# Optimization experiments

Measured on AMD Instinct MI355X. Metric: run time of the kernel, lower is better.

## Reference

```python
import jax, jax.numpy as jnp
import numpy as np

B, M, N, Z = 4, 64, 64, 64
IN_DIM, OUT_DIM = 32, 32
MODES1 = MODES2 = MODES3 = 16
HIDDEN = OUT_DIM * 4  # factor=4, n_ff_layers=2
LN_EPS = 1e-5


def setup_inputs() -> dict:
    key = jax.random.key(0)
    ks = jax.random.split(key, 10)
    # xavier-normal-ish scale for (in, out, modes, 2) fourier weights
    fscale = np.sqrt(2.0 / (IN_DIM + OUT_DIM))
    x = jax.random.normal(ks[0], (B, M, N, Z, IN_DIM), dtype=jnp.float32)
    wx = jax.random.normal(ks[1], (IN_DIM, OUT_DIM, MODES1, 2), dtype=jnp.float32) * fscale
    wy = jax.random.normal(ks[2], (IN_DIM, OUT_DIM, MODES2, 2), dtype=jnp.float32) * fscale
    wz = jax.random.normal(ks[3], (IN_DIM, OUT_DIM, MODES3, 2), dtype=jnp.float32) * fscale
    # FeedForward: Linear(OUT_DIM, HIDDEN) + ReLU, then Linear(HIDDEN, OUT_DIM) + LayerNorm
    w0 = jax.random.normal(ks[4], (OUT_DIM, HIDDEN), dtype=jnp.float32) * np.sqrt(1.0 / OUT_DIM)
    b0 = jnp.zeros((HIDDEN,), dtype=jnp.float32)
    w1 = jax.random.normal(ks[5], (HIDDEN, OUT_DIM), dtype=jnp.float32) * np.sqrt(1.0 / HIDDEN)
    b1 = jnp.zeros((OUT_DIM,), dtype=jnp.float32)
    ln_g = jnp.ones((OUT_DIM,), dtype=jnp.float32)
    ln_b = jnp.zeros((OUT_DIM,), dtype=jnp.float32)
    return {"x": x, "wx": wx, "wy": wy, "wz": wz,
            "w0": w0, "b0": b0, "w1": w1, "b1": b1,
            "ln_g": ln_g, "ln_b": ln_b}


def _as_complex(w):
    return w[..., 0] + 1j * w[..., 1]


def _forward_fourier(x, wx, wy, wz):
    # x: [b, m, n, z, i] -> [b, i, m, n, z]
    xt = jnp.transpose(x, (0, 4, 1, 2, 3))
    # --- axis M (dim 2) ---
    ftx = jnp.fft.rfft(xt, axis=2, norm='ortho')  # [b, i, M//2+1, n, z] complex
    ox = jnp.einsum('bixyz,iox->boxyz', ftx[:, :, :MODES1], _as_complex(wx))
    ox = jnp.pad(ox, ((0, 0), (0, 0), (0, M // 2 + 1 - MODES1), (0, 0), (0, 0)))
    xx = jnp.fft.irfft(ox, n=M, axis=2, norm='ortho')
    # --- axis N (dim 3) ---
    fty = jnp.fft.rfft(xt, axis=3, norm='ortho')
    oy = jnp.einsum('bixyz,ioy->boxyz', fty[:, :, :, :MODES2], _as_complex(wy))
    oy = jnp.pad(oy, ((0, 0), (0, 0), (0, 0), (0, N // 2 + 1 - MODES2), (0, 0)))
    xy = jnp.fft.irfft(oy, n=N, axis=3, norm='ortho')
    # --- axis Z (dim 4) ---
    ftz = jnp.fft.rfft(xt, axis=4, norm='ortho')
    oz = jnp.einsum('bixyz,ioz->boxyz', ftz[:, :, :, :, :MODES3], _as_complex(wz))
    oz = jnp.pad(oz, ((0, 0), (0, 0), (0, 0), (0, 0), (0, Z // 2 + 1 - MODES3)))
    xz = jnp.fft.irfft(oz, n=Z, axis=4, norm='ortho')
    out = xx + xy + xz  # [b, o, m, n, z]
    return jnp.transpose(out, (0, 2, 3, 4, 1))  # [b, m, n, z, o]


def reference(x, wx, wy, wz, w0, b0, w1, b1, ln_g, ln_b):
    s = _forward_fourier(x, wx, wy, wz)
    h = jax.nn.relu(s @ w0 + b0)
    y = h @ w1 + b1
    mu = jnp.mean(y, axis=-1, keepdims=True)
    var = jnp.mean((y - mu) ** 2, axis=-1, keepdims=True)
    y = (y - mu) * jax.lax.rsqrt(var + LN_EPS) * ln_g + ln_b
    return y
```

## Files before the change

### kernel.cpp

```cpp
#include <hip/hip_runtime.h>
#include <math.h>

typedef __attribute__((ext_vector_type(8))) short short8v;
typedef __attribute__((ext_vector_type(4))) float float4v;

constexpr float THETA = 6.28318530717958647692f / 64.0f;

constexpr int S_B = 64 * 64 * 64 * 32;
constexpr int S_M = 64 * 64 * 32;
constexpr int S_N = 64 * 32;
constexpr int S_Z = 32;

__device__ __forceinline__ unsigned short f2bf(float f) {
    unsigned int u = __builtin_bit_cast(unsigned int, f);
    u += 0x7FFFu + ((u >> 16) & 1u);
    return (unsigned short)(u >> 16);
}

constexpr int WS_TF = 98304, WS_TI = 100352, WS_TOTAL = 102400;

__global__ __launch_bounds__(256)
void setup_frags(const float* __restrict__ wx, const float* __restrict__ wy,
                 const float* __restrict__ wz, unsigned short* __restrict__ W)
{
    int f0 = (blockIdx.x * 256 + threadIdx.x) * 4;
#pragma unroll
    for (int u = 0; u < 4; ++u) {
        int f = f0 + u;
        if (f >= WS_TOTAL) continue;
        unsigned short v;
        if (f < WS_TF) {
            int ax = f >> 15, rem = f & 32767;
            int k = rem >> 11;
            int rem2 = rem & 2047;
            int wt = rem2 >> 10, rt = (rem2 >> 9) & 1, l = (rem2 >> 3) & 63, e = rem2 & 7;
            int o = 16 * rt + (l & 15), i = 8 * (l >> 4) + e;
            const float* w = (ax == 0) ? wx : ((ax == 1) ? wy : wz);
            v = f2bf(w[((i * 32 + o) * 16 + k) * 2 + wt]);
        } else if (f < WS_TI) {
            int rem = f - WS_TF;
            int jt = rem >> 10, s = (rem >> 9) & 1, l = (rem >> 3) & 63, e = rem & 7;
            int kk = l & 15, m = 32 * s + 8 * (l >> 4) + e;
            int jm = (kk * m) & 63;
            float ang = THETA * (float)jm;
            v = f2bf(jt == 0 ? cosf(ang) : sinf(ang));
        } else {
            int rem = f - WS_TI;
            int mt = rem >> 9, l = (rem >> 3) & 63, e = rem & 7;
            int mp = 16 * mt + (l & 15), r = 8 * (l >> 4) + e;
            int k = r & 15;
            float sk = (k == 0) ? (1.0f / 64.0f) : (2.0f / 64.0f);
            int jm = (k * mp) & 63;
            float ang = THETA * (float)jm;
            v = f2bf(r < 16 ? sk * cosf(ang) : -sk * sinf(ang));
        }
        W[f] = v;
    }
}

constexpr int AB_SHORTS = 8192;
__device__ __forceinline__ int ab8(int t, int k, int line, int i) {
    return ((((t * 16 + k) * 8 + line) * 64) + i * 2) ^ (((line ^ k) & 7) << 4);
}
constexpr int P_LS = 1288;
constexpr int P_SHORTS = 8 * P_LS;
__device__ __forceinline__ int p8(int line, int o, int r) {
    return line * P_LS + o * 40 + r;
}

template <int STRIDE>
__device__ __forceinline__ void stageF(const float* __restrict__ x,
                                       const long* base2,
                                       const unsigned short* __restrict__ tf,
                                       unsigned short* __restrict__ AB,
                                       int lane, int wave)
{
    const int gq = lane >> 4, c = lane & 15;
    short8v tfB[2][2];
#pragma unroll
    for (int jt = 0; jt < 2; ++jt)
#pragma unroll
        for (int s = 0; s < 2; ++s)
            tfB[jt][s] = *reinterpret_cast<const short8v*>(tf + ((jt * 2 + s) * 64 + lane) * 8);

#pragma unroll
    for (int li = 0; li < 2; ++li) {
        const int line = wave * 2 + li;
        float4v acc[2][2];
#pragma unroll
        for (int rt = 0; rt < 2; ++rt)
#pragma unroll
            for (int jt = 0; jt < 2; ++jt)
                acc[rt][jt] = float4v{0.f, 0.f, 0.f, 0.f};

#pragma unroll
        for (int rt = 0; rt < 2; ++rt) {
            const float* xp = x + base2[li] + 16 * rt + c;
#pragma unroll
            for (int s = 0; s < 2; ++s) {
                short8v a;
#pragma unroll
                for (int e = 0; e < 8; ++e)
                    a[e] = (short)f2bf(xp[(long)(32 * s + 8 * gq + e) * STRIDE]);
                acc[rt][0] = __builtin_amdgcn_mfma_f32_16x16x32_bf16(a, tfB[0][s], acc[rt][0], 0, 0, 0);
                acc[rt][1] = __builtin_amdgcn_mfma_f32_16x16x32_bf16(a, tfB[1][s], acc[rt][1], 0, 0, 0);
            }
        }
#pragma unroll
        for (int rt = 0; rt < 2; ++rt)
#pragma unroll
            for (int jt = 0; jt < 2; ++jt) {
                unsigned int lo = (unsigned int)f2bf(acc[rt][jt][0]) | ((unsigned int)f2bf(acc[rt][jt][1]) << 16);
                unsigned int hi = (unsigned int)f2bf(acc[rt][jt][2]) | ((unsigned int)f2bf(acc[rt][jt][3]) << 16);
                *reinterpret_cast<uint2*>(reinterpret_cast<char*>(AB) + ab8(jt, c, line, 16 * rt + 4 * gq)) =
                    make_uint2(lo, hi);
            }
    }
}

__device__ __forceinline__ void stageMx(const unsigned short* __restrict__ wf,
                                        const unsigned short* __restrict__ AB,
                                        unsigned short* __restrict__ P,
                                        int lane, int wave)
{
    const int gq = lane >> 4, c = lane & 15;
    const int t2 = wave >> 1, rt = wave & 1, lc = c & 7;
    for (int k = 0; k < 16; k += 2) {
        float4v acc2[2];
#pragma unroll
        for (int kk = 0; kk < 2; ++kk) {
            const int kc = k + kk;
            short8v aT = *reinterpret_cast<const short8v*>(reinterpret_cast<const char*>(AB) + ab8(0, kc, lc, 8 * gq));
            short8v bT = *reinterpret_cast<const short8v*>(reinterpret_cast<const char*>(AB) + ab8(1, kc, lc, 8 * gq));
            const int w1t = t2 ? 1 : 0, w2t = t2 ? 0 : 1;
            short8v w1 = *reinterpret_cast<const short8v*>(wf + (((kc * 2 + w1t) * 2 + rt) * 64 + lane) * 8);
            short8v w2 = *reinterpret_cast<const short8v*>(wf + (((kc * 2 + w2t) * 2 + rt) * 64 + lane) * 8);
            if (t2) {
                union { short8v s; unsigned int u[4]; } nb;
                nb.s = bT;
#pragma unroll
                for (int j = 0; j < 4; ++j) nb.u[j] ^= 0x80008000u;
                bT = nb.s;
            }
            float4v a2 = float4v{0.f, 0.f, 0.f, 0.f};
            a2 = __builtin_amdgcn_mfma_f32_16x16x32_bf16(w1, aT, a2, 0, 0, 0);
            a2 = __builtin_amdgcn_mfma_f32_16x16x32_bf16(w2, bT, a2, 0, 0, 0);
            acc2[kk] = a2;
        }
        if (c < 8) {
#pragma unroll
            for (int r = 0; r < 4; ++r) {
                unsigned int u = (unsigned int)f2bf(acc2[0][r]) | ((unsigned int)f2bf(acc2[1][r]) << 16);
                *reinterpret_cast<unsigned int*>(&P[p8(c, 16 * rt + 4 * gq + r, 16 * t2 + k)]) = u;
            }
        }
    }
}

template <int AXIS, bool ACCUM>
__global__ __launch_bounds__(256)
void spectral_mfma(const float* __restrict__ x,
                   const unsigned short* __restrict__ wf,
                   const unsigned short* __restrict__ tf,
                   const unsigned short* __restrict__ ti,
                   float* __restrict__ out)
{
    __shared__ __align__(16) unsigned short AB[AB_SHORTS];
    __shared__ __align__(16) unsigned short P[P_SHORTS];

    const int t = threadIdx.x, lane = t & 63, wave = t >> 6;
    const int gq = lane >> 4, c = lane & 15;
    constexpr int stride = (AXIS == 0) ? S_M : S_N;
    const int l0 = blockIdx.x * 8;

    long base2[2];
#pragma unroll
    for (int li = 0; li < 2; ++li) {
        int l = l0 + wave * 2 + li;
        int b = l >> 12, p1 = (l >> 6) & 63, p2 = l & 63;
        base2[li] = (AXIS == 0)
            ? (long)b * S_B + (long)p1 * S_N + (long)p2 * S_Z
            : (long)b * S_B + (long)p1 * S_M + (long)p2 * S_Z;
    }

    stageF<stride>(x, base2, tf, AB, lane, wave);
    __syncthreads();
    stageMx(wf, AB, P, lane, wave);
    __syncthreads();

    short8v tiB[4];
#pragma unroll
    for (int mt = 0; mt < 4; ++mt)
        tiB[mt] = *reinterpret_cast<const short8v*>(ti + (mt * 64 + lane) * 8);

#pragma unroll
    for (int li = 0; li < 2; ++li) {
        const int line = wave * 2 + li;
        short8v pA[2];
        pA[0] = *reinterpret_cast<const short8v*>(&P[p8(line, c, 8 * gq)]);
        pA[1] = *reinterpret_cast<const short8v*>(&P[p8(line, 16 + c, 8 * gq)]);
#pragma unroll
        for (int rt = 0; rt < 2; ++rt)
#pragma unroll
            for (int mt = 0; mt < 4; ++mt) {
                float4v acc = float4v{0.f, 0.f, 0.f, 0.f};
                acc = __builtin_amdgcn_mfma_f32_16x16x32_bf16(pA[rt], tiB[mt], acc, 0, 0, 0);
                float* op = out + base2[li] + (long)(16 * mt + c) * stride + 16 * rt + 4 * gq;
                if (ACCUM) {
                    float4 old = *reinterpret_cast<const float4*>(op);
                    old.x += acc[0]; old.y += acc[1]; old.z += acc[2]; old.w += acc[3];
                    *reinterpret_cast<float4*>(op) = old;
                } else {
                    *reinterpret_cast<float4*>(op) = make_float4(acc[0], acc[1], acc[2], acc[3]);
                }
            }
    }
}

__global__ __launch_bounds__(256)
void spectral_fused(const float* __restrict__ x,
                    const unsigned short* __restrict__ wf,
                    const unsigned short* __restrict__ tf,
                    const unsigned short* __restrict__ ti,
                    const float* __restrict__ w0, const float* __restrict__ b0,
                    const float* __restrict__ w1, const float* __restrict__ b1,
                    const float* __restrict__ g,  const float* __restrict__ bb,
                    float* __restrict__ out)
{
    __shared__ __align__(16) unsigned short sm[38976];
    constexpr int OP = 8192, OS = 18496;

    const int t = threadIdx.x, lane = t & 63, wave = t >> 6;
    const int gq = lane >> 4, c = lane & 15;
    const int l0 = blockIdx.x * 8;

    long base2[2];
#pragma unroll
    for (int li = 0; li < 2; ++li) {
        int l = l0 + wave * 2 + li;
        int b = l >> 12, p1 = (l >> 6) & 63, p2 = l & 63;
        base2[li] = (long)b * S_B + (long)p1 * S_M + (long)p2 * S_N;
    }

    float b0v[8], b1v[2], gv[2], bvv[2];
#pragma unroll
    for (int n = 0; n < 8; ++n) b0v[n] = b0[n * 16 + c];
#pragma unroll
    for (int n = 0; n < 2; ++n) { b1v[n] = b1[n * 16 + c]; gv[n] = g[n * 16 + c]; bvv[n] = bb[n * 16 + c]; }

    stageF<S_Z>(x, base2, tf, sm, lane, wave);
    __syncthreads();
    stageMx(wf, sm, sm + OP, lane, wave);
    __syncthreads();

    for (int s = t; s < 512; s += 256) {
        const int n = s >> 6, ln = s & 63, g2 = ln >> 4, c2 = ln & 15;
        const int kb = n >> 1, nn = n & 1;
        short8v v0, v1;
#pragma unroll
        for (int e = 0; e < 8; ++e) {
            v0[e] = (short)f2bf(w0[(8 * g2 + e) * 128 + n * 16 + c2]);
            v1[e] = (short)f2bf(w1[(32 * kb + 8 * g2 + e) * 32 + nn * 16 + c2]);
        }
        *reinterpret_cast<short8v*>(&sm[s * 8])        = v0;
        *reinterpret_cast<short8v*>(&sm[4096 + s * 8]) = v1;
    }

    short8v tiB[4];
#pragma unroll
    for (int mt = 0; mt < 4; ++mt)
        tiB[mt] = *reinterpret_cast<const short8v*>(ti + (mt * 64 + lane) * 8);

#pragma unroll
    for (int li = 0; li < 2; ++li) {
        const int line = wave * 2 + li;
        const long bs = base2[li];
        short8v pA[2];
        pA[0] = *reinterpret_cast<const short8v*>(&sm[OP + p8(line, c, 8 * gq)]);
        pA[1] = *reinterpret_cast<const short8v*>(&sm[OP + p8(line, 16 + c, 8 * gq)]);
#pragma unroll
        for (int rt = 0; rt < 2; ++rt)
#pragma unroll
            for (int mt = 0; mt < 4; ++mt) {
                float4v acc = float4v{0.f, 0.f, 0.f, 0.f};
                acc = __builtin_amdgcn_mfma_f32_16x16x32_bf16(pA[rt], tiB[mt], acc, 0, 0, 0);
                const float* op = out + bs + (long)(16 * mt + c) * S_Z + 16 * rt + 4 * gq;
                float4 old = *reinterpret_cast<const float4*>(op);
                const float v0 = old.x + acc[0], v1 = old.y + acc[1];
                const float v2 = old.z + acc[2], v3 = old.w + acc[3];
                const int si = OS + (line * 64 + 16 * mt + c) * 40 + 16 * rt + 4 * gq;
                *reinterpret_cast<unsigned int*>(&sm[si])     = (unsigned int)f2bf(v0) | ((unsigned int)f2bf(v1) << 16);
                *reinterpret_cast<unsigned int*>(&sm[si + 2]) = (unsigned int)f2bf(v2) | ((unsigned int)f2bf(v3) << 16);
            }
    }
    __syncthreads();

    const int Hb = OP + wave * 2560;
#pragma unroll
    for (int li = 0; li < 2; ++li) {
        const int line = wave * 2 + li;
        const long bs = base2[li];

        short8v af[4];
#pragma unroll
        for (int f = 0; f < 4; ++f)
            af[f] = *reinterpret_cast<const short8v*>(&sm[OS + (line * 64 + 16 * f + c) * 40 + 8 * gq]);

        float4v Y[4][2];
#pragma unroll
        for (int f = 0; f < 4; ++f)
#pragma unroll
            for (int n = 0; n < 2; ++n)
                Y[f][n] = float4v{b1v[n], b1v[n], b1v[n], b1v[n]};

#pragma unroll
        for (int kb = 0; kb < 4; ++kb) {
#pragma unroll
            for (int nn = 0; nn < 2; ++nn) {
                const int n = 2 * kb + nn;
                const short8v wv = *reinterpret_cast<const short8v*>(&sm[(n * 64 + lane) * 8]);
#pragma unroll
                for (int f = 0; f < 4; ++f) {
                    float4v hacc = float4v{b0v[n], b0v[n], b0v[n], b0v[n]};
                    hacc = __builtin_amdgcn_mfma_f32_16x16x32_bf16(af[f], wv, hacc, 0, 0, 0);
#pragma unroll
                    for (int r = 0; r < 4; ++r)
                        sm[Hb + (16 * f + 4 * gq + r) * 40 + nn * 16 + c] = f2bf(fmaxf(hacc[r], 0.f));
                }
            }
            const short8v wva = *reinterpret_cast<const short8v*>(&sm[4096 + ((kb * 2 + 0) * 64 + lane) * 8]);
            const short8v wvb = *reinterpret_cast<const short8v*>(&sm[4096 + ((kb * 2 + 1) * 64 + lane) * 8]);
#pragma unroll
            for (int f = 0; f < 4; ++f) {
                const short8v a2 = *reinterpret_cast<const short8v*>(&sm[Hb + (16 * f + c) * 40 + 8 * gq]);
                Y[f][0] = __builtin_amdgcn_mfma_f32_16x16x32_bf16(a2, wva, Y[f][0], 0, 0, 0);
                Y[f][1] = __builtin_amdgcn_mfma_f32_16x16x32_bf16(a2, wvb, Y[f][1], 0, 0, 0);
            }
        }

#pragma unroll
        for (int f = 0; f < 4; ++f) {
            float smv[4], sq[4];
#pragma unroll
            for (int r = 0; r < 4; ++r) {
                const float v0 = Y[f][0][r], v1 = Y[f][1][r];
                smv[r] = v0 + v1;
                sq[r]  = v0 * v0 + v1 * v1;
            }
#pragma unroll
            for (int mask = 1; mask <= 8; mask <<= 1) {
#pragma unroll
                for (int r = 0; r < 4; ++r) {
                    smv[r] += __shfl_xor(smv[r], mask);
                    sq[r]  += __shfl_xor(sq[r], mask);
                }
            }
#pragma unroll
            for (int r = 0; r < 4; ++r) {
                const float mu = smv[r] * (1.0f / 32.0f);
                const float var = sq[r] * (1.0f / 32.0f) - mu * mu;
                const float rs = rsqrtf(var + 1e-5f);
                float* op = out + bs + (long)(16 * f + 4 * gq + r) * 32;
                op[c]      = (Y[f][0][r] - mu) * rs * gv[0] + bvv[0];
                op[16 + c] = (Y[f][1][r] - mu) * rs * gv[1] + bvv[1];
            }
        }
    }
}

extern "C" void kernel_launch(void* const* d_in, const int* in_sizes, int n_in,
                              void* d_out, int out_size, void* d_ws, size_t ws_size,
                              hipStream_t stream)
{
    const float* x    = (const float*)d_in[0];
    const float* wx   = (const float*)d_in[1];
    const float* wy   = (const float*)d_in[2];
    const float* wz   = (const float*)d_in[3];
    const float* w0   = (const float*)d_in[4];
    const float* b0   = (const float*)d_in[5];
    const float* w1   = (const float*)d_in[6];
    const float* b1   = (const float*)d_in[7];
    const float* ln_g = (const float*)d_in[8];
    const float* ln_b = (const float*)d_in[9];
    float* out = (float*)d_out;

    unsigned short* wsf = (unsigned short*)d_ws;

    setup_frags<<<100, 256, 0, stream>>>(wx, wy, wz, wsf);

    spectral_mfma<0, false><<<2048, 256, 0, stream>>>(x, wsf + 0 * 32768, wsf + WS_TF, wsf + WS_TI, out);
    spectral_mfma<1, true ><<<2048, 256, 0, stream>>>(x, wsf + 1 * 32768, wsf + WS_TF, wsf + WS_TI, out);
    spectral_fused<<<2048, 256, 0, stream>>>(x, wsf + 2 * 32768, wsf + WS_TF, wsf + WS_TI,
                                             w0, b0, w1, b1, ln_g, ln_b, out);
}
```

Before: 260.8 us.

## Store spectral partial sums in bf16 workspace and halve lines per block

The first two axis kernels now write and accumulate their partial results as bf16 in a workspace buffer instead of fp32 in the output, halving the bytes moved for the intermediate sum. This only happens when the workspace is large enough; otherwise the old fp32 path is used. Each block now handles 4 lines (one per wave) instead of 8, doubling the grid to 4096 blocks and shrinking shared memory per block to raise occupancy. The bf16 intermediate adds rounding error to the summed spectral output.

```diff
diff --git a/kernel.cpp b/kernel.cpp
--- a/kernel.cpp
+++ b/kernel.cpp
@@ -15,6 +15,9 @@
     unsigned int u = __builtin_bit_cast(unsigned int, f);
     u += 0x7FFFu + ((u >> 16) & 1u);
     return (unsigned short)(u >> 16);
+}
+__device__ __forceinline__ float bf2f(unsigned int h) {
+    return __builtin_bit_cast(float, h << 16);
 }
 
 constexpr int WS_TF = 98304, WS_TI = 100352, WS_TOTAL = 102400;
@@ -58,22 +61,21 @@
     }
 }
 
-constexpr int AB_SHORTS = 8192;
-__device__ __forceinline__ int ab8(int t, int k, int line, int i) {
-    return ((((t * 16 + k) * 8 + line) * 64) + i * 2) ^ (((line ^ k) & 7) << 4);
+constexpr int AB_SHORTS = 4096;
+__device__ __forceinline__ int ab4(int t, int k, int line, int i) {
+    return ((((t * 16 + k) * 4 + line) * 64) + i * 2) ^ (((line ^ k) & 7) << 4);
 }
 constexpr int P_LS = 1288;
-constexpr int P_SHORTS = 8 * P_LS;
-__device__ __forceinline__ int p8(int line, int o, int r) {
+constexpr int P_SHORTS = 4 * P_LS;
+__device__ __forceinline__ int p4(int line, int o, int r) {
     return line * P_LS + o * 40 + r;
 }
 
 template <int STRIDE>
-__device__ __forceinline__ void stageF(const float* __restrict__ x,
-                                       const long* base2,
-                                       const unsigned short* __restrict__ tf,
-                                       unsigned short* __restrict__ AB,
-                                       int lane, int wave)
+__device__ __forceinline__ void stageF1(const float* __restrict__ x, long bs,
+                                        const unsigned short* __restrict__ tf,
+                                        unsigned short* __restrict__ AB,
+                                        int lane, int line)
 {
     const int gq = lane >> 4, c = lane & 15;
     short8v tfB[2][2];
@@ -83,55 +85,51 @@
         for (int s = 0; s < 2; ++s)
             tfB[jt][s] = *reinterpret_cast<const short8v*>(tf + ((jt * 2 + s) * 64 + lane) * 8);
 
-#pragma unroll
-    for (int li = 0; li < 2; ++li) {
-        const int line = wave * 2 + li;
-        float4v acc[2][2];
-#pragma unroll
-        for (int rt = 0; rt < 2; ++rt)
-#pragma unroll
-            for (int jt = 0; jt < 2; ++jt)
-                acc[rt][jt] = float4v{0.f, 0.f, 0.f, 0.f};
-
-#pragma unroll
-        for (int rt = 0; rt < 2; ++rt) {
-            const float* xp = x + base2[li] + 16 * rt + c;
-#pragma unroll
-            for (int s = 0; s < 2; ++s) {
-                short8v a;
-#pragma unroll
-                for (int e = 0; e < 8; ++e)
-                    a[e] = (short)f2bf(xp[(long)(32 * s + 8 * gq + e) * STRIDE]);
-                acc[rt][0] = __builtin_amdgcn_mfma_f32_16x16x32_bf16(a, tfB[0][s], acc[rt][0], 0, 0, 0);
-                acc[rt][1] = __builtin_amdgcn_mfma_f32_16x16x32_bf16(a, tfB[1][s], acc[rt][1], 0, 0, 0);
-            }
-        }
-#pragma unroll
-        for (int rt = 0; rt < 2; ++rt)
-#pragma unroll
-            for (int jt = 0; jt < 2; ++jt) {
-                unsigned int lo = (unsigned int)f2bf(acc[rt][jt][0]) | ((unsigned int)f2bf(acc[rt][jt][1]) << 16);
-                unsigned int hi = (unsigned int)f2bf(acc[rt][jt][2]) | ((unsigned int)f2bf(acc[rt][jt][3]) << 16);
-                *reinterpret_cast<uint2*>(reinterpret_cast<char*>(AB) + ab8(jt, c, line, 16 * rt + 4 * gq)) =
-                    make_uint2(lo, hi);
-            }
-    }
-}
-
-__device__ __forceinline__ void stageMx(const unsigned short* __restrict__ wf,
-                                        const unsigned short* __restrict__ AB,
-                                        unsigned short* __restrict__ P,
-                                        int lane, int wave)
+    float4v acc[2][2];
+#pragma unroll
+    for (int rt = 0; rt < 2; ++rt)
+#pragma unroll
+        for (int jt = 0; jt < 2; ++jt)
+            acc[rt][jt] = float4v{0.f, 0.f, 0.f, 0.f};
+
+#pragma unroll
+    for (int rt = 0; rt < 2; ++rt) {
+        const float* xp = x + bs + 16 * rt + c;
+#pragma unroll
+        for (int s = 0; s < 2; ++s) {
+            short8v a;
+#pragma unroll
+            for (int e = 0; e < 8; ++e)
+                a[e] = (short)f2bf(xp[(long)(32 * s + 8 * gq + e) * STRIDE]);
+            acc[rt][0] = __builtin_amdgcn_mfma_f32_16x16x32_bf16(a, tfB[0][s], acc[rt][0], 0, 0, 0);
+            acc[rt][1] = __builtin_amdgcn_mfma_f32_16x16x32_bf16(a, tfB[1][s], acc[rt][1], 0, 0, 0);
+        }
+    }
+#pragma unroll
+    for (int rt = 0; rt < 2; ++rt)
+#pragma unroll
+        for (int jt = 0; jt < 2; ++jt) {
+            unsigned int lo = (unsigned int)f2bf(acc[rt][jt][0]) | ((unsigned int)f2bf(acc[rt][jt][1]) << 16);
+            unsigned int hi = (unsigned int)f2bf(acc[rt][jt][2]) | ((unsigned int)f2bf(acc[rt][jt][3]) << 16);
+            *reinterpret_cast<uint2*>(reinterpret_cast<char*>(AB) + ab4(jt, c, line, 16 * rt + 4 * gq)) =
+                make_uint2(lo, hi);
+        }
+}
+
+__device__ __forceinline__ void stageMx4(const unsigned short* __restrict__ wf,
+                                         const unsigned short* __restrict__ AB,
+                                         unsigned short* __restrict__ P,
+                                         int lane, int wave)
 {
     const int gq = lane >> 4, c = lane & 15;
-    const int t2 = wave >> 1, rt = wave & 1, lc = c & 7;
+    const int t2 = wave >> 1, rt = wave & 1, lc = c & 3;
     for (int k = 0; k < 16; k += 2) {
         float4v acc2[2];
 #pragma unroll
         for (int kk = 0; kk < 2; ++kk) {
             const int kc = k + kk;
-            short8v aT = *reinterpret_cast<const short8v*>(reinterpret_cast<const char*>(AB) + ab8(0, kc, lc, 8 * gq));
-            short8v bT = *reinterpret_cast<const short8v*>(reinterpret_cast<const char*>(AB) + ab8(1, kc, lc, 8 * gq));
+            short8v aT = *reinterpret_cast<const short8v*>(reinterpret_cast<const char*>(AB) + ab4(0, kc, lc, 8 * gq));
+            short8v bT = *reinterpret_cast<const short8v*>(reinterpret_cast<const char*>(AB) + ab4(1, kc, lc, 8 * gq));
             const int w1t = t2 ? 1 : 0, w2t = t2 ? 0 : 1;
             short8v w1 = *reinterpret_cast<const short8v*>(wf + (((kc * 2 + w1t) * 2 + rt) * 64 + lane) * 8);
             short8v w2 = *reinterpret_cast<const short8v*>(wf + (((kc * 2 + w2t) * 2 + rt) * 64 + lane) * 8);
@@ -147,23 +145,24 @@
             a2 = __builtin_amdgcn_mfma_f32_16x16x32_bf16(w2, bT, a2, 0, 0, 0);
             acc2[kk] = a2;
         }
-        if (c < 8) {
+        if (c < 4) {
 #pragma unroll
             for (int r = 0; r < 4; ++r) {
                 unsigned int u = (unsigned int)f2bf(acc2[0][r]) | ((unsigned int)f2bf(acc2[1][r]) << 16);
-                *reinterpret_cast<unsigned int*>(&P[p8(c, 16 * rt + 4 * gq + r, 16 * t2 + k)]) = u;
-            }
-        }
-    }
-}
-
-template <int AXIS, bool ACCUM>
+                *reinterpret_cast<unsigned int*>(&P[p4(c, 16 * rt + 4 * gq + r, 16 * t2 + k)]) = u;
+            }
+        }
+    }
+}
+
+template <int AXIS, int MODE>
 __global__ __launch_bounds__(256)
 void spectral_mfma(const float* __restrict__ x,
                    const unsigned short* __restrict__ wf,
                    const unsigned short* __restrict__ tf,
                    const unsigned short* __restrict__ ti,
-                   float* __restrict__ out)
+                   float* __restrict__ out,
+                   unsigned short* __restrict__ pw)
 {
     __shared__ __align__(16) unsigned short AB[AB_SHORTS];
     __shared__ __align__(16) unsigned short P[P_SHORTS];
@@ -171,21 +170,16 @@
     const int t = threadIdx.x, lane = t & 63, wave = t >> 6;
     const int gq = lane >> 4, c = lane & 15;
     constexpr int stride = (AXIS == 0) ? S_M : S_N;
-    const int l0 = blockIdx.x * 8;
-
-    long base2[2];
-#pragma unroll
-    for (int li = 0; li < 2; ++li) {
-        int l = l0 + wave * 2 + li;
-        int b = l >> 12, p1 = (l >> 6) & 63, p2 = l & 63;
-        base2[li] = (AXIS == 0)
-            ? (long)b * S_B + (long)p1 * S_N + (long)p2 * S_Z
-            : (long)b * S_B + (long)p1 * S_M + (long)p2 * S_Z;
-    }
-
-    stageF<stride>(x, base2, tf, AB, lane, wave);
+
+    const int l = blockIdx.x * 4 + wave;
+    const int b = l >> 12, p1 = (l >> 6) & 63, p2 = l & 63;
+    const long bs = (AXIS == 0)
+        ? (long)b * S_B + (long)p1 * S_N + (long)p2 * S_Z
+        : (long)b * S_B + (long)p1 * S_M + (long)p2 * S_Z;
+
+    stageF1<stride>(x, bs, tf, AB, lane, wave);
     __syncthreads();
-    stageMx(wf, AB, P, lane, wave);
+    stageMx4(wf, AB, P, lane, wave);
     __syncthreads();
 
     short8v tiB[4];
@@ -193,30 +187,43 @@
     for (int mt = 0; mt < 4; ++mt)
         tiB[mt] = *reinterpret_cast<const short8v*>(ti + (mt * 64 + lane) * 8);
 
-#pragma unroll
-    for (int li = 0; li < 2; ++li) {
-        const int line = wave * 2 + li;
-        short8v pA[2];
-        pA[0] = *reinterpret_cast<const short8v*>(&P[p8(line, c, 8 * gq)]);
-        pA[1] = *reinterpret_cast<const short8v*>(&P[p8(line, 16 + c, 8 * gq)]);
-#pragma unroll
-        for (int rt = 0; rt < 2; ++rt)
-#pragma unroll
-            for (int mt = 0; mt < 4; ++mt) {
-                float4v acc = float4v{0.f, 0.f, 0.f, 0.f};
-                acc = __builtin_amdgcn_mfma_f32_16x16x32_bf16(pA[rt], tiB[mt], acc, 0, 0, 0);
-                float* op = out + base2[li] + (long)(16 * mt + c) * stride + 16 * rt + 4 * gq;
-                if (ACCUM) {
-                    float4 old = *reinterpret_cast<const float4*>(op);
-                    old.x += acc[0]; old.y += acc[1]; old.z += acc[2]; old.w += acc[3];
-                    *reinterpret_cast<float4*>(op) = old;
-                } else {
-                    *reinterpret_cast<float4*>(op) = make_float4(acc[0], acc[1], acc[2], acc[3]);
-                }
-            }
-    }
-}
-
+    short8v pA[2];
+    pA[0] = *reinterpret_cast<const short8v*>(&P[p4(wave, c, 8 * gq)]);
+    pA[1] = *reinterpret_cast<const short8v*>(&P[p4(wave, 16 + c, 8 * gq)]);
+
+#pragma unroll
+    for (int rt = 0; rt < 2; ++rt)
+#pragma unroll
+        for (int mt = 0; mt < 4; ++mt) {
+            float4v acc = float4v{0.f, 0.f, 0.f, 0.f};
+            acc = __builtin_amdgcn_mfma_f32_16x16x32_bf16(pA[rt], tiB[mt], acc, 0, 0, 0);
+            const long off = bs + (long)(16 * mt + c) * stride + 16 * rt + 4 * gq;
+            if (MODE == 0) {
+                *reinterpret_cast<float4*>(out + off) = make_float4(acc[0], acc[1], acc[2], acc[3]);
+            } else if (MODE == 1) {
+                float4 old = *reinterpret_cast<const float4*>(out + off);
+                old.x += acc[0]; old.y += acc[1]; old.z += acc[2]; old.w += acc[3];
+                *reinterpret_cast<float4*>(out + off) = old;
+            } else if (MODE == 2) {
+                uint2 pv;
+                pv.x = (unsigned int)f2bf(acc[0]) | ((unsigned int)f2bf(acc[1]) << 16);
+                pv.y = (unsigned int)f2bf(acc[2]) | ((unsigned int)f2bf(acc[3]) << 16);
+                *reinterpret_cast<uint2*>(pw + off) = pv;
+            } else {
+                uint2 old = *reinterpret_cast<const uint2*>(pw + off);
+                const float v0 = bf2f(old.x & 0xffffu) + acc[0];
+                const float v1 = bf2f(old.x >> 16)     + acc[1];
+                const float v2 = bf2f(old.y & 0xffffu) + acc[2];
+                const float v3 = bf2f(old.y >> 16)     + acc[3];
+                uint2 pv;
+                pv.x = (unsigned int)f2bf(v0) | ((unsigned int)f2bf(v1) << 16);
+                pv.y = (unsigned int)f2bf(v2) | ((unsigned int)f2bf(v3) << 16);
+                *reinterpret_cast<uint2*>(pw + off) = pv;
+            }
+        }
+}
+
+template <bool BF16P>
 __global__ __launch_bounds__(256)
 void spectral_fused(const float* __restrict__ x,
                     const unsigned short* __restrict__ wf,
@@ -225,22 +232,18 @@
                     const float* __restrict__ w0, const float* __restrict__ b0,
                     const float* __restrict__ w1, const float* __restrict__ b1,
                     const float* __restrict__ g,  const float* __restrict__ bb,
+                    const void* __restrict__ partial,
                     float* __restrict__ out)
 {
-    __shared__ __align__(16) unsigned short sm[38976];
-    constexpr int OP = 8192, OS = 18496;
+    __shared__ __align__(16) unsigned short sm[23584];
+    constexpr int OP = 8192, OS = 13344;
 
     const int t = threadIdx.x, lane = t & 63, wave = t >> 6;
     const int gq = lane >> 4, c = lane & 15;
-    const int l0 = blockIdx.x * 8;
-
-    long base2[2];
-#pragma unroll
-    for (int li = 0; li < 2; ++li) {
-        int l = l0 + wave * 2 + li;
-        int b = l >> 12, p1 = (l >> 6) & 63, p2 = l & 63;
-        base2[li] = (long)b * S_B + (long)p1 * S_M + (long)p2 * S_N;
-    }
+
+    const int l = blockIdx.x * 4 + wave;
+    const int b = l >> 12, p1 = (l >> 6) & 63, p2 = l & 63;
+    const long bs = (long)b * S_B + (long)p1 * S_M + (long)p2 * S_N;
 
     float b0v[8], b1v[2], gv[2], bvv[2];
 #pragma unroll
@@ -248,9 +251,9 @@
 #pragma unroll
     for (int n = 0; n < 2; ++n) { b1v[n] = b1[n * 16 + c]; gv[n] = g[n * 16 + c]; bvv[n] = bb[n * 16 + c]; }
 
-    stageF<S_Z>(x, base2, tf, sm, lane, wave);
+    stageF1<S_Z>(x, bs, tf, sm, lane, wave);
     __syncthreads();
-    stageMx(wf, sm, sm + OP, lane, wave);
+    stageMx4(wf, sm, sm + OP, lane, wave);
     __syncthreads();
 
     for (int s = t; s < 512; s += 256) {
@@ -271,99 +274,100 @@
     for (int mt = 0; mt < 4; ++mt)
         tiB[mt] = *reinterpret_cast<const short8v*>(ti + (mt * 64 + lane) * 8);
 
-#pragma unroll
-    for (int li = 0; li < 2; ++li) {
-        const int line = wave * 2 + li;
-        const long bs = base2[li];
+    {
         short8v pA[2];
-        pA[0] = *reinterpret_cast<const short8v*>(&sm[OP + p8(line, c, 8 * gq)]);
-        pA[1] = *reinterpret_cast<const short8v*>(&sm[OP + p8(line, 16 + c, 8 * gq)]);
+        pA[0] = *reinterpret_cast<const short8v*>(&sm[OP + p4(wave, c, 8 * gq)]);
+        pA[1] = *reinterpret_cast<const short8v*>(&sm[OP + p4(wave, 16 + c, 8 * gq)]);
 #pragma unroll
         for (int rt = 0; rt < 2; ++rt)
 #pragma unroll
             for (int mt = 0; mt < 4; ++mt) {
                 float4v acc = float4v{0.f, 0.f, 0.f, 0.f};
                 acc = __builtin_amdgcn_mfma_f32_16x16x32_bf16(pA[rt], tiB[mt], acc, 0, 0, 0);
-                const float* op = out + bs + (long)(16 * mt + c) * S_Z + 16 * rt + 4 * gq;
-                float4 old = *reinterpret_cast<const float4*>(op);
-                const float v0 = old.x + acc[0], v1 = old.y + acc[1];
-                const float v2 = old.z + acc[2], v3 = old.w + acc[3];
-                const int si = OS + (line * 64 + 16 * mt + c) * 40 + 16 * rt + 4 * gq;
+                const long off = bs + (long)(16 * mt + c) * S_Z + 16 * rt + 4 * gq;
+                float v0, v1, v2, v3;
+                if (BF16P) {
+                    uint2 pv = *reinterpret_cast<const uint2*>((const unsigned short*)partial + off);
+                    v0 = bf2f(pv.x & 0xffffu) + acc[0];
+                    v1 = bf2f(pv.x >> 16)     + acc[1];
+                    v2 = bf2f(pv.y & 0xffffu) + acc[2];
+                    v3 = bf2f(pv.y >> 16)     + acc[3];
+                } else {
+                    float4 old = *reinterpret_cast<const float4*>((const float*)partial + off);
+                    v0 = old.x + acc[0]; v1 = old.y + acc[1];
+                    v2 = old.z + acc[2]; v3 = old.w + acc[3];
+                }
+                const int si = OS + (wave * 64 + 16 * mt + c) * 40 + 16 * rt + 4 * gq;
                 *reinterpret_cast<unsigned int*>(&sm[si])     = (unsigned int)f2bf(v0) | ((unsigned int)f2bf(v1) << 16);
                 *reinterpret_cast<unsigned int*>(&sm[si + 2]) = (unsigned int)f2bf(v2) | ((unsigned int)f2bf(v3) << 16);
             }
     }
     __syncthreads();
 
-    const int Hb = OP + wave * 2560;
-#pragma unroll
-    for (int li = 0; li < 2; ++li) {
-        const int line = wave * 2 + li;
-        const long bs = base2[li];
-
-        short8v af[4];
-#pragma unroll
-        for (int f = 0; f < 4; ++f)
-            af[f] = *reinterpret_cast<const short8v*>(&sm[OS + (line * 64 + 16 * f + c) * 40 + 8 * gq]);
-
-        float4v Y[4][2];
-#pragma unroll
-        for (int f = 0; f < 4; ++f)
-#pragma unroll
-            for (int n = 0; n < 2; ++n)
-                Y[f][n] = float4v{b1v[n], b1v[n], b1v[n], b1v[n]};
-
-#pragma unroll
-        for (int kb = 0; kb < 4; ++kb) {
-#pragma unroll
-            for (int nn = 0; nn < 2; ++nn) {
-                const int n = 2 * kb + nn;
-                const short8v wv = *reinterpret_cast<const short8v*>(&sm[(n * 64 + lane) * 8]);
-#pragma unroll
-                for (int f = 0; f < 4; ++f) {
-                    float4v hacc = float4v{b0v[n], b0v[n], b0v[n], b0v[n]};
-                    hacc = __builtin_amdgcn_mfma_f32_16x16x32_bf16(af[f], wv, hacc, 0, 0, 0);
-#pragma unroll
-                    for (int r = 0; r < 4; ++r)
-                        sm[Hb + (16 * f + 4 * gq + r) * 40 + nn * 16 + c] = f2bf(fmaxf(hacc[r], 0.f));
-                }
-            }
-            const short8v wva = *reinterpret_cast<const short8v*>(&sm[4096 + ((kb * 2 + 0) * 64 + lane) * 8]);
-            const short8v wvb = *reinterpret_cast<const short8v*>(&sm[4096 + ((kb * 2 + 1) * 64 + lane) * 8]);
+    const int Hb = OS + wave * 2560;
+
+    short8v af[4];
+#pragma unroll
+    for (int f = 0; f < 4; ++f)
+        af[f] = *reinterpret_cast<const short8v*>(&sm[OS + (wave * 64 + 16 * f + c) * 40 + 8 * gq]);
+
+    float4v Y[4][2];
+#pragma unroll
+    for (int f = 0; f < 4; ++f)
+#pragma unroll
+        for (int n = 0; n < 2; ++n)
+            Y[f][n] = float4v{b1v[n], b1v[n], b1v[n], b1v[n]};
+
+#pragma unroll
+    for (int kb = 0; kb < 4; ++kb) {
+#pragma unroll
+        for (int nn = 0; nn < 2; ++nn) {
+            const int n = 2 * kb + nn;
+            const short8v wv = *reinterpret_cast<const short8v*>(&sm[(n * 64 + lane) * 8]);
 #pragma unroll
             for (int f = 0; f < 4; ++f) {
-                const short8v a2 = *reinterpret_cast<const short8v*>(&sm[Hb + (16 * f + c) * 40 + 8 * gq]);
-                Y[f][0] = __builtin_amdgcn_mfma_f32_16x16x32_bf16(a2, wva, Y[f][0], 0, 0, 0);
-                Y[f][1] = __builtin_amdgcn_mfma_f32_16x16x32_bf16(a2, wvb, Y[f][1], 0, 0, 0);
-            }
-        }
-
+                float4v hacc = float4v{b0v[n], b0v[n], b0v[n], b0v[n]};
+                hacc = __builtin_amdgcn_mfma_f32_16x16x32_bf16(af[f], wv, hacc, 0, 0, 0);
+#pragma unroll
+                for (int r = 0; r < 4; ++r)
+                    sm[Hb + (16 * f + 4 * gq + r) * 40 + nn * 16 + c] = f2bf(fmaxf(hacc[r], 0.f));
+            }
+        }
+        const short8v wva = *reinterpret_cast<const short8v*>(&sm[4096 + ((kb * 2 + 0) * 64 + lane) * 8]);
+        const short8v wvb = *reinterpret_cast<const short8v*>(&sm[4096 + ((kb * 2 + 1) * 64 + lane) * 8]);
 #pragma unroll
         for (int f = 0; f < 4; ++f) {
-            float smv[4], sq[4];
+            const short8v a2 = *reinterpret_cast<const short8v*>(&sm[Hb + (16 * f + c) * 40 + 8 * gq]);
+            Y[f][0] = __builtin_amdgcn_mfma_f32_16x16x32_bf16(a2, wva, Y[f][0], 0, 0, 0);
+            Y[f][1] = __builtin_amdgcn_mfma_f32_16x16x32_bf16(a2, wvb, Y[f][1], 0, 0, 0);
+        }
+    }
+
+#pragma unroll
+    for (int f = 0; f < 4; ++f) {
+        float smv[4], sq[4];
+#pragma unroll
+        for (int r = 0; r < 4; ++r) {
+            const float v0 = Y[f][0][r], v1 = Y[f][1][r];
+            smv[r] = v0 + v1;
+            sq[r]  = v0 * v0 + v1 * v1;
+        }
+#pragma unroll
+        for (int mask = 1; mask <= 8; mask <<= 1) {
 #pragma unroll
             for (int r = 0; r < 4; ++r) {
-                const float v0 = Y[f][0][r], v1 = Y[f][1][r];
-                smv[r] = v0 + v1;
-                sq[r]  = v0 * v0 + v1 * v1;
-            }
-#pragma unroll
-            for (int mask = 1; mask <= 8; mask <<= 1) {
-#pragma unroll
-                for (int r = 0; r < 4; ++r) {
-                    smv[r] += __shfl_xor(smv[r], mask);
-                    sq[r]  += __shfl_xor(sq[r], mask);
-                }
-            }
-#pragma unroll
-            for (int r = 0; r < 4; ++r) {
-                const float mu = smv[r] * (1.0f / 32.0f);
-                const float var = sq[r] * (1.0f / 32.0f) - mu * mu;
-                const float rs = rsqrtf(var + 1e-5f);
-                float* op = out + bs + (long)(16 * f + 4 * gq + r) * 32;
-                op[c]      = (Y[f][0][r] - mu) * rs * gv[0] + bvv[0];
-                op[16 + c] = (Y[f][1][r] - mu) * rs * gv[1] + bvv[1];
-            }
+                smv[r] += __shfl_xor(smv[r], mask);
+                sq[r]  += __shfl_xor(sq[r], mask);
+            }
+        }
+#pragma unroll
+        for (int r = 0; r < 4; ++r) {
+            const float mu = smv[r] * (1.0f / 32.0f);
+            const float var = sq[r] * (1.0f / 32.0f) - mu * mu;
+            const float rs = rsqrtf(var + 1e-5f);
+            float* op = out + bs + (long)(16 * f + 4 * gq + r) * 32;
+            op[c]      = (Y[f][0][r] - mu) * rs * gv[0] + bvv[0];
+            op[16 + c] = (Y[f][1][r] - mu) * rs * gv[1] + bvv[1];
         }
     }
 }
@@ -386,10 +390,22 @@
 
     unsigned short* wsf = (unsigned short*)d_ws;
 
+    const size_t PART_OFF   = 262144;
+    const size_t PART_BYTES = (size_t)33554432 * 2;
+    const bool bf16p = ws_size >= PART_OFF + PART_BYTES;
+    unsigned short* pw = (unsigned short*)((char*)d_ws + PART_OFF);
+
     setup_frags<<<100, 256, 0, stream>>>(wx, wy, wz, wsf);
 
-    spectral_mfma<0, false><<<2048, 256, 0, stream>>>(x, wsf + 0 * 32768, wsf + WS_TF, wsf + WS_TI, out);
-    spectral_mfma<1, true ><<<2048, 256, 0, stream>>>(x, wsf + 1 * 32768, wsf + WS_TF, wsf + WS_TI, out);
-    spectral_fused<<<2048, 256, 0, stream>>>(x, wsf + 2 * 32768, wsf + WS_TF, wsf + WS_TI,
-                                             w0, b0, w1, b1, ln_g, ln_b, out);
-}
+    if (bf16p) {
+        spectral_mfma<0, 2><<<4096, 256, 0, stream>>>(x, wsf + 0 * 32768, wsf + WS_TF, wsf + WS_TI, out, pw);
+        spectral_mfma<1, 3><<<4096, 256, 0, stream>>>(x, wsf + 1 * 32768, wsf + WS_TF, wsf + WS_TI, out, pw);
+        spectral_fused<true><<<4096, 256, 0, stream>>>(x, wsf + 2 * 32768, wsf + WS_TF, wsf + WS_TI,
+                                                       w0, b0, w1, b1, ln_g, ln_b, pw, out);
+    } else {
+        spectral_mfma<0, 0><<<4096, 256, 0, stream>>>(x, wsf + 0 * 32768, wsf + WS_TF, wsf + WS_TI, out, pw);
+        spectral_mfma<1, 1><<<4096, 256, 0, stream>>>(x, wsf + 1 * 32768, wsf + WS_TF, wsf + WS_TI, out, pw);
+        spectral_fused<false><<<4096, 256, 0, stream>>>(x, wsf + 2 * 32768, wsf + WS_TF, wsf + WS_TI,
+                                                        w0, b0, w1, b1, ln_g, ln_b, out, out);
+    }
+}
```

After: 229.1 us. 12.2% less time.
